# Optimization experiments

Measured on AMD Instinct MI355X. Metric: run time of the kernel, lower is better.

The kernel has to match this reference:

```python
import jax, jax.numpy as jnp
import numpy as np

N = 100000      # num_nodes
R = 8           # num_relations
D = 128         # hidden_dim
E = 600000      # num_edges
P = 100000      # num query pairs
PH = 128        # pair_hidden_dim


def _xavier(key, shape):
    fan_in, fan_out = shape[-2], shape[-1]
    limit = float(np.sqrt(6.0 / (fan_in + fan_out)))
    return jax.random.uniform(key, shape, jnp.float32, -limit, limit)


def setup_inputs() -> dict:
    key = jax.random.key(0)
    ks = jax.random.split(key, 16)
    edge_index = jax.random.randint(ks[0], (2, E), 0, N)
    edge_type = jax.random.randint(ks[1], (E,), 0, R)
    drug_index = jax.random.randint(ks[2], (P,), 0, N)
    disease_index = jax.random.randint(ks[3], (P,), 0, N)
    emb = _xavier(ks[4], (N, D))
    rw1 = _xavier(ks[5], (R, D, D))
    sl1 = _xavier(ks[6], (D, D))
    b1 = jnp.zeros((D,), jnp.float32)
    rw2 = _xavier(ks[7], (R, D, D))
    sl2 = _xavier(ks[8], (D, D))
    b2 = jnp.zeros((D,), jnp.float32)
    pw1 = _xavier(ks[9], (3 * D, PH))
    pb1 = jnp.zeros((PH,), jnp.float32)
    pw2 = _xavier(ks[10], (PH, 1))
    pb2 = jnp.zeros((1,), jnp.float32)
    return {
        "edge_index": edge_index, "edge_type": edge_type,
        "drug_index": drug_index, "disease_index": disease_index,
        "emb": emb, "rw1": rw1, "sl1": sl1, "b1": b1,
        "rw2": rw2, "sl2": sl2, "b2": b2,
        "pw1": pw1, "pb1": pb1, "pw2": pw2, "pb2": pb2,
    }


def _rgcn_layer(x, rel_w, self_w, bias, src, dst, etype):
    # Transform all node features once per relation: [R, N, D]
    xW = jnp.einsum('nd,rde->rne', x, rel_w)
    # Per-relation in-degree of dst (matches torch bincount-per-relation, clamp_min(1))
    seg_key = etype * N + dst                                  # [E]
    deg = jax.ops.segment_sum(jnp.ones((src.shape[0],), x.dtype), seg_key,
                              num_segments=R * N)
    deg = jnp.maximum(deg, 1.0)
    msg = xW[etype, src] / deg[seg_key][:, None]               # [E, D]
    agg = jax.ops.segment_sum(msg, dst, num_segments=N)        # [N, D]
    return x @ self_w + agg + bias


def reference(edge_index, edge_type, drug_index, disease_index,
              emb, rw1, sl1, b1, rw2, sl2, b2, pw1, pb1, pw2, pb2):
    src, dst = edge_index[0], edge_index[1]
    # encode (eval mode: dropout is identity)
    x = _rgcn_layer(emb, rw1, sl1, b1, src, dst, edge_type)
    x = jax.nn.relu(x)
    x = _rgcn_layer(x, rw2, sl2, b2, src, dst, edge_type)
    # score_pairs
    dh = x[drug_index]
    sh = x[disease_index]
    feat = jnp.concatenate((dh, sh, dh * sh), axis=-1)         # [P, 3D]
    h = jax.nn.relu(feat @ pw1 + pb1)
    logits = (h @ pw2 + pb2)[:, 0]                             # [P]
    return logits
```

## Files before the change

### kernel.cpp

```cpp
#include <hip/hip_runtime.h>

#define D 128
#define RMAX 16

typedef short s16x8 __attribute__((ext_vector_type(8)));
typedef float f32x4 __attribute__((ext_vector_type(4)));

__device__ inline unsigned short f2b(float f) {
    unsigned u = __builtin_bit_cast(unsigned, f);
    unsigned r = (u + 0x7FFFu + ((u >> 16) & 1u)) >> 16;
    return (unsigned short)r;
}
__device__ inline float b2f(unsigned short h) {
    unsigned u = ((unsigned)h) << 16;
    return __builtin_bit_cast(float, u);
}


__global__ void k_count2(const int* __restrict__ etype, const int* __restrict__ srcA,
                         const int* __restrict__ dstA, int E, int N, int R,
                         int* __restrict__ deg, int* __restrict__ srcCnt,
                         int* __restrict__ counts) {
    __shared__ int lh[RMAX];
    if (threadIdx.x < RMAX) lh[threadIdx.x] = 0;
    __syncthreads();
    int e = blockIdx.x * blockDim.x + threadIdx.x;
    if (e < E) {
        int r = etype[e];
        atomicAdd(&deg[r * N + dstA[e]], 1);
        atomicAdd(&srcCnt[r * N + srcA[e]], 1);
        atomicAdd(&lh[r], 1);
    }
    __syncthreads();
    if (threadIdx.x < R && lh[threadIdx.x])
        atomicAdd(&counts[threadIdx.x], lh[threadIdx.x]);
}

__global__ void k_offsets(const int* __restrict__ counts, int* __restrict__ po,
                          int R, int N) {
    if (threadIdx.x == 0 && blockIdx.x == 0) {
        int acc = 0;
        for (int r = 0; r < R; ++r) {
            po[r] = acc;
            acc += ((counts[r] + 127) / 128) * 128;
        }
        po[R] = acc;
        acc += ((N + 127) / 128) * 128;
        po[R + 1] = acc;
    }
}


template<int VPT>
__global__ void k_scan_blk(const int* __restrict__ in, int* __restrict__ tmp,
                           int* __restrict__ bsum, int n) {
    __shared__ int sd[256];
    int t = threadIdx.x;
    long base = (long)blockIdx.x * (256 * VPT) + (long)t * VPT;
    int s[VPT];
    int tsum = 0;
    #pragma unroll
    for (int k = 0; k < VPT; ++k) { s[k] = (base + k < n) ? in[base + k] : 0; tsum += s[k]; }
    sd[t] = tsum;
    __syncthreads();
    for (int off = 1; off < 256; off <<= 1) {
        int v = (t >= off) ? sd[t - off] : 0;
        __syncthreads();
        sd[t] += v;
        __syncthreads();
    }
    int run = sd[t] - tsum;
    #pragma unroll
    for (int k = 0; k < VPT; ++k) { if (base + k < n) tmp[base + k] = run; run += s[k]; }
    if (t == 255) bsum[blockIdx.x] = sd[255];
}

__global__ void k_scanD1(const int* __restrict__ deg, int* __restrict__ tmp,
                         int* __restrict__ bsum, int N, int R) {
    __shared__ int sd[256];
    int t = threadIdx.x;
    long base = (long)blockIdx.x * 1024 + (long)t * 4;
    int s[4];
    int tsum = 0;
    #pragma unroll
    for (int k = 0; k < 4; ++k) {
        int v = 0;
        long d = base + k;
        if (d < N) {
            v = 1;
            for (int r = 0; r < R; ++r) v += deg[(size_t)r * N + d];
        }
        s[k] = v; tsum += v;
    }
    sd[t] = tsum;
    __syncthreads();
    for (int off = 1; off < 256; off <<= 1) {
        int v = (t >= off) ? sd[t - off] : 0;
        __syncthreads();
        sd[t] += v;
        __syncthreads();
    }
    int run = sd[t] - tsum;
    #pragma unroll
    for (int k = 0; k < 4; ++k) { if (base + k < N) tmp[base + k] = run; run += s[k]; }
    if (t == 255) bsum[blockIdx.x] = sd[255];
}

__global__ void k_scan2(const int* __restrict__ bsum, int* __restrict__ boff, int nb,
                        int* __restrict__ tail, int tailval) {
    __shared__ int sd[256];
    int t = threadIdx.x;
    int v = (t < nb) ? bsum[t] : 0;
    sd[t] = v;
    __syncthreads();
    for (int off = 1; off < 256; off <<= 1) {
        int w = (t >= off) ? sd[t - off] : 0;
        __syncthreads();
        sd[t] += w;
        __syncthreads();
    }
    if (t < nb) boff[t] = sd[t] - v;
    if (t == 0 && tail) *tail = tailval;
}

__global__ void k_scan3(const int* __restrict__ tmp, const int* __restrict__ boff,
                        int* __restrict__ out, int n, int shift) {
    int i = blockIdx.x * 256 + threadIdx.x;
    if (i < n) out[i] = tmp[i] + boff[i >> shift];
}


__global__ void k_scatter3(const int* __restrict__ etype, const int* __restrict__ srcA,
                           const int* __restrict__ dstA, int E, int N, int R,
                           const int* __restrict__ srcOff, const int* __restrict__ po,
                           const int* __restrict__ rowstart, const int* __restrict__ deg,
                           int* __restrict__ srcCur, int* __restrict__ cur2,
                           int* __restrict__ slotSrc, float* __restrict__ slotScale,
                           int* __restrict__ red_idx) {
    int t = blockIdx.x * 256 + threadIdx.x;
    if (t < E) {
        int r = etype[t];
        int s = srcA[t], d = dstA[t];
        int bin = r * N + s;
        int rank = atomicAdd(&srcCur[bin], 1);
        int pos = po[r] + (srcOff[bin] - srcOff[r * N]) + rank;
        int rank2 = atomicAdd(&cur2[d], 1);
        slotSrc[pos] = s;
        slotScale[pos] = 1.0f / (float)deg[r * N + d];
        red_idx[rowstart[d] + 1 + rank2] = pos;
    } else if (t < E + N) {
        int n = t - E;
        int pos = po[R] + n;
        slotSrc[pos] = n;
        slotScale[pos] = 1.0f;
        red_idx[rowstart[n]] = pos;
    }
}


__global__ void k_prep(const float* __restrict__ emb,
                       const float* __restrict__ rw1, const float* __restrict__ sl1,
                       const float* __restrict__ rw2, const float* __restrict__ sl2,
                       const float* __restrict__ pw1,
                       unsigned short* __restrict__ embb,
                       unsigned short* __restrict__ wAll1,
                       unsigned short* __restrict__ wAll2,
                       unsigned short* __restrict__ pw1T,
                       int N, int R)
{
    long t = (long)blockIdx.x * 256 + threadIdx.x;
    long u0 = (long)N * D / 4;
    if (t < u0) {
        long i = t * 4;
        f32x4 v = *(const f32x4*)(emb + i);
        unsigned a0 = (unsigned)f2b(v[0]) | ((unsigned)f2b(v[1]) << 16);
        unsigned a1 = (unsigned)f2b(v[2]) | ((unsigned)f2b(v[3]) << 16);
        uint2 o; o.x = a0; o.y = a1;
        *(uint2*)(embb + i) = o;
        return;
    }
    t -= u0;
    long uW = (long)(R + 1) * D * D;
    if (t < 2 * uW) {
        const float* rw = (t < uW) ? rw1 : rw2;
        const float* sl = (t < uW) ? sl1 : sl2;
        unsigned short* o = (t < uW) ? wAll1 : wAll2;
        long u = (t < uW) ? t : t - uW;
        int r = (int)(u >> 14);
        int nb = (int)(u & 16383);
        int n = nb >> 7, kk = nb & 127;
        int ke = kk ^ ((n & 7) << 3);
        float v = (r < R) ? rw[((size_t)r * D + ke) * D + n] : sl[(size_t)ke * D + n];
        o[u] = f2b(v);
        return;
    }
    t -= 2 * uW;
    if (t < 3 * D * D) {
        int n = (int)(t / 384), ck = (int)(t - n * 384);
        int ch = ck >> 7, kl = (ck & 127) ^ ((n & 7) << 3);
        pw1T[t] = f2b(pw1[(size_t)(ch * 128 + kl) * 128 + n]);
    }
}


__global__ __launch_bounds__(256) void k_gemm_msg(
    const unsigned short* __restrict__ xb,
    const unsigned short* __restrict__ wAll,
    const int* __restrict__ slotSrc, const float* __restrict__ slotScale,
    const int* __restrict__ po, int R,
    unsigned short* __restrict__ y)
{
    __shared__ unsigned char smB[32768];
    __shared__ float sscale[128];
    int tid = threadIdx.x;
    int row0 = blockIdx.x * 128;
    if (row0 >= po[R + 1]) return;
    int r = 0;
    while (row0 >= po[r + 1]) ++r;

    int lane = tid & 63, wid = tid >> 6;
    int lo = lane & 15, hi = lane >> 4;

    int r0g = wid * 32 + lo, r1g = r0g + 16;
    int sv0 = slotSrc[row0 + r0g];
    int sv1 = slotSrc[row0 + r1g];
    const unsigned short* xrow0 = xb + (size_t)sv0 * D;
    const unsigned short* xrow1 = xb + (size_t)sv1 * D;
    s16x8 a0[4], a1[4];
    #pragma unroll
    for (int ks = 0; ks < 4; ++ks) {
        a0[ks] = *(const s16x8*)(xrow0 + ks * 32 + hi * 8);
        a1[ks] = *(const s16x8*)(xrow1 + ks * 32 + hi * 8);
    }

    if (tid < 128) sscale[tid] = slotScale[row0 + tid];

    {
        const int4* src = (const int4*)(wAll + (size_t)r * D * D);
        int4* dstl = (int4*)smB;
        #pragma unroll
        for (int i = 0; i < 8; ++i) dstl[tid + i * 256] = src[tid + i * 256];
    }
    __syncthreads();

    f32x4 acc[2][8];
    #pragma unroll
    for (int a = 0; a < 2; ++a)
        #pragma unroll
        for (int b = 0; b < 8; ++b) acc[a][b] = (f32x4){0, 0, 0, 0};

    #pragma unroll
    for (int ks = 0; ks < 4; ++ks) {
        int kb = ks * 64 + hi * 16;
        #pragma unroll
        for (int n = 0; n < 8; ++n) {
            int cr = n * 16 + lo;
            s16x8 bf = *(const s16x8*)(smB + cr * 256 + (kb ^ ((cr & 7) << 4)));
            acc[0][n] = __builtin_amdgcn_mfma_f32_16x16x32_bf16(a0[ks], bf, acc[0][n], 0, 0, 0);
            acc[1][n] = __builtin_amdgcn_mfma_f32_16x16x32_bf16(a1[ks], bf, acc[1][n], 0, 0, 0);
        }
    }

    __syncthreads();
    #pragma unroll
    for (int m2 = 0; m2 < 2; ++m2) {
        int rbase = wid * 32 + m2 * 16 + hi * 4;
        #pragma unroll
        for (int reg = 0; reg < 4; ++reg) {
            int rl = rbase + reg;
            float s = sscale[rl];
            #pragma unroll
            for (int n = 0; n < 8; ++n) {
                int byteoff = rl * 256 + (((n * 32 + (lo >> 3) * 16) ^ ((rl & 7) << 4)) + (lo & 7) * 2);
                *(unsigned short*)(smB + byteoff) = f2b(acc[m2][n][reg] * s);
            }
        }
    }
    __syncthreads();
    {
        int m = tid >> 1, half = tid & 1;
        unsigned short* dst = y + (size_t)(row0 + m) * D;
        #pragma unroll
        for (int i = 0; i < 8; ++i) {
            int c = half * 8 + i;
            int4 v = *(const int4*)(smB + m * 256 + ((c * 16) ^ ((m & 7) << 4)));
            *(int4*)(dst + c * 8) = v;
        }
    }
}


template<bool RELU>
__global__ void k_reduce(const unsigned short* __restrict__ y,
                         const int* __restrict__ red_idx,
                         const int* __restrict__ rowstart,
                         const float* __restrict__ bias,
                         unsigned short* __restrict__ out, int N)
{
    int tid = threadIdx.x;
    int dl = tid >> 4, cj = tid & 15;
    float b[8];
    *(f32x4*)(b)     = *(const f32x4*)(bias + cj * 8);
    *(f32x4*)(b + 4) = *(const f32x4*)(bias + cj * 8 + 4);
    int dbase = blockIdx.x * 64 + dl * 4;
    for (int i = 0; i < 4; ++i) {
        int d = dbase + i;
        if (d >= N) return;
        int s = rowstart[d], e = rowstart[d + 1];
        float a[8];
        #pragma unroll
        for (int j = 0; j < 8; ++j) a[j] = b[j];
        for (int q = s; q < e; ++q) {
            int pos = red_idx[q];
            int4 v = *(const int4*)(y + (size_t)pos * D + cj * 8);
            const unsigned short* hp = (const unsigned short*)&v;
            #pragma unroll
            for (int j = 0; j < 8; ++j) a[j] += b2f(hp[j]);
        }
        unsigned short o[8];
        #pragma unroll
        for (int j = 0; j < 8; ++j) {
            float v = RELU ? fmaxf(a[j], 0.0f) : a[j];
            o[j] = f2b(v);
        }
        *(int4*)(out + (size_t)d * D + cj * 8) = *(const int4*)o;
    }
}


__global__ __launch_bounds__(256) void k_score(
    const unsigned short* __restrict__ x2b,
    const int* __restrict__ drug, const int* __restrict__ dis,
    const unsigned short* __restrict__ pw1T,
    const float* __restrict__ pb1, const float* __restrict__ pw2,
    const float* __restrict__ pb2, float* __restrict__ outp, int P)
{
    __shared__ unsigned char smA[32768];
    __shared__ unsigned char smB[32768];
    __shared__ float pb1s[128];
    __shared__ float pw2s[128];
    int tid = threadIdx.x;
    long p0 = (long)blockIdx.x * 128;
    if (tid < 128) { pb1s[tid] = pb1[tid]; pw2s[tid] = pw2[tid]; }
    float pb2v = pb2[0];

    int lane = tid & 63, wid = tid >> 6;
    int lo = lane & 15, hi = lane >> 4;
    f32x4 acc[2][8];
    #pragma unroll
    for (int a = 0; a < 2; ++a)
        #pragma unroll
        for (int b = 0; b < 8; ++b) acc[a][b] = (f32x4){0, 0, 0, 0};

    for (int ch = 0; ch < 3; ++ch) {
        {
            const int4* src = (const int4*)pw1T;
            int4* dstl = (int4*)smB;
            #pragma unroll
            for (int i = 0; i < 8; ++i) {
                int q = tid + i * 256;
                int n = q >> 4, c = q & 15;
                dstl[q] = src[n * 48 + ch * 16 + c];
            }
        }
        {
            int m = tid >> 1, half = tid & 1;
            long p = p0 + m;
            int4 z = {0, 0, 0, 0};
            if (p < P) {
                const int4* da = (const int4*)(x2b + (size_t)drug[p] * D);
                const int4* db = (const int4*)(x2b + (size_t)dis[p] * D);
                for (int c = half * 8; c < half * 8 + 8; ++c) {
                    int4 v;
                    if (ch == 0) v = da[c];
                    else if (ch == 1) v = db[c];
                    else {
                        int4 va = da[c], vb = db[c];
                        const unsigned short* ap = (const unsigned short*)&va;
                        const unsigned short* bp = (const unsigned short*)&vb;
                        unsigned short o[8];
                        #pragma unroll
                        for (int j = 0; j < 8; ++j) o[j] = f2b(b2f(ap[j]) * b2f(bp[j]));
                        v = *(const int4*)o;
                    }
                    *(int4*)(smA + m * 256 + ((c * 16) ^ ((m & 7) << 4))) = v;
                }
            } else {
                for (int c = half * 8; c < half * 8 + 8; ++c)
                    *(int4*)(smA + m * 256 + ((c * 16) ^ ((m & 7) << 4))) = z;
            }
        }
        __syncthreads();

        #pragma unroll
        for (int ks = 0; ks < 4; ++ks) {
            int kb = ks * 64 + hi * 16;
            int r0 = wid * 32 + lo, r1 = r0 + 16;
            s16x8 a0 = *(const s16x8*)(smA + r0 * 256 + (kb ^ ((r0 & 7) << 4)));
            s16x8 a1 = *(const s16x8*)(smA + r1 * 256 + (kb ^ ((r1 & 7) << 4)));
            #pragma unroll
            for (int n = 0; n < 8; ++n) {
                int cr = n * 16 + lo;
                s16x8 bf = *(const s16x8*)(smB + cr * 256 + (kb ^ ((cr & 7) << 4)));
                acc[0][n] = __builtin_amdgcn_mfma_f32_16x16x32_bf16(a0, bf, acc[0][n], 0, 0, 0);
                acc[1][n] = __builtin_amdgcn_mfma_f32_16x16x32_bf16(a1, bf, acc[1][n], 0, 0, 0);
            }
        }
        __syncthreads();
    }

    #pragma unroll
    for (int m2 = 0; m2 < 2; ++m2)
        #pragma unroll
        for (int reg = 0; reg < 4; ++reg) {
            float s = 0.0f;
            #pragma unroll
            for (int n = 0; n < 8; ++n) {
                int col = n * 16 + lo;
                float v = acc[m2][n][reg] + pb1s[col];
                v = fmaxf(v, 0.0f);
                s = fmaf(v, pw2s[col], s);
            }
            s += __shfl_xor(s, 1, 64);
            s += __shfl_xor(s, 2, 64);
            s += __shfl_xor(s, 4, 64);
            s += __shfl_xor(s, 8, 64);
            long p = p0 + wid * 32 + m2 * 16 + hi * 4 + reg;
            if (lo == 0 && p < P) outp[p] = s + pb2v;
        }
}


extern "C" void kernel_launch(void* const* d_in, const int* in_sizes, int n_in,
                              void* d_out, int out_size, void* d_ws, size_t ws_size,
                              hipStream_t stream) {
    const int*   edge_index = (const int*)d_in[0];
    const int*   edge_type  = (const int*)d_in[1];
    const int*   drug       = (const int*)d_in[2];
    const int*   dis        = (const int*)d_in[3];
    const float* emb        = (const float*)d_in[4];
    const float* rw1        = (const float*)d_in[5];
    const float* sl1        = (const float*)d_in[6];
    const float* b1         = (const float*)d_in[7];
    const float* rw2        = (const float*)d_in[8];
    const float* sl2        = (const float*)d_in[9];
    const float* b2         = (const float*)d_in[10];
    const float* pw1        = (const float*)d_in[11];
    const float* pb1        = (const float*)d_in[12];
    const float* pw2        = (const float*)d_in[13];
    const float* pb2        = (const float*)d_in[14];

    const int E = in_sizes[1];
    const int P = in_sizes[2];
    const int N = in_sizes[4] / D;
    const int R = in_sizes[5] / (D * D);

    const int* srcA = edge_index;
    const int* dstA = edge_index + E;

    const int slotN = E + N + 128 * (R + 1);

    char* ws = (char*)d_ws;
    unsigned short* embb = (unsigned short*)ws; ws += (size_t)N * D * 2;
    unsigned short* x1b  = (unsigned short*)ws; ws += (size_t)N * D * 2;
    unsigned short* y    = (unsigned short*)ws; ws += (size_t)slotN * D * 2;
    unsigned short* wAll1 = (unsigned short*)ws; ws += (size_t)(R + 1) * D * D * 2;
    unsigned short* wAll2 = (unsigned short*)ws; ws += (size_t)(R + 1) * D * D * 2;
    unsigned short* pw1T  = (unsigned short*)ws; ws += (size_t)3 * D * D * 2;
    int*   deg     = (int*)ws;   ws += (size_t)R * N * 4;
    int*   srcCnt  = (int*)ws;   ws += (size_t)R * N * 4;
    int*   srcCur  = (int*)ws;   ws += (size_t)R * N * 4;
    int*   cur2    = (int*)ws;   ws += (size_t)N * 4;
    int*   counts  = (int*)ws;   ws += 256;
    int*   slotSrc = (int*)ws;   ws += (size_t)slotN * 4;
    float* slotScale = (float*)ws; ws += (size_t)slotN * 4;
    size_t zbytes = (size_t)(3 * R * N + N + 64 + 2 * slotN) * 4;
    int*   red_idx = (int*)ws;   ws += (size_t)(E + N) * 4;
    int* srcOff  = (int*)ws; ws += (size_t)R * N * 4;
    int* dtmp    = (int*)ws; ws += (size_t)N * 4;
    int* rowstart = (int*)ws; ws += (size_t)(N + 1) * 4;
    int* bsumS   = (int*)ws; ws += 256 * 4;
    int* boffS   = (int*)ws; ws += 256 * 4;
    int* bsumD   = (int*)ws; ws += 256 * 4;
    int* boffD   = (int*)ws; ws += 256 * 4;
    int* po      = (int*)ws; ws += 256;
    unsigned short* x2b = embb;

    hipMemsetAsync(deg, 0, zbytes, stream);

    long u0 = (long)N * D / 4;
    long uW = (long)(R + 1) * D * D;
    long utot = u0 + 2 * uW + 3 * D * D;
    k_prep<<<(int)((utot + 255) / 256), 256, 0, stream>>>(emb, rw1, sl1, rw2, sl2, pw1,
                                                          embb, wAll1, wAll2, pw1T, N, R);

    k_count2<<<(E + 255) / 256, 256, 0, stream>>>(edge_type, srcA, dstA, E, N, R,
                                                  deg, srcCnt, counts);
    k_offsets<<<1, 1, 0, stream>>>(counts, po, R, N);

    int nbS = (R * N + 4095) / 4096;
    k_scan_blk<16><<<nbS, 256, 0, stream>>>(srcCnt, srcOff, bsumS, R * N);
    k_scan2<<<1, 256, 0, stream>>>(bsumS, boffS, nbS, nullptr, 0);
    k_scan3<<<(R * N + 255) / 256, 256, 0, stream>>>(srcOff, boffS, srcOff, R * N, 12);

    int nbD = (N + 1023) / 1024;
    k_scanD1<<<nbD, 256, 0, stream>>>(deg, dtmp, bsumD, N, R);
    k_scan2<<<1, 256, 0, stream>>>(bsumD, boffD, nbD, rowstart + N, E + N);
    k_scan3<<<(N + 255) / 256, 256, 0, stream>>>(dtmp, boffD, rowstart, N, 10);

    k_scatter3<<<(E + N + 255) / 256, 256, 0, stream>>>(edge_type, srcA, dstA, E, N, R,
                                                        srcOff, po, rowstart, deg,
                                                        srcCur, cur2,
                                                        slotSrc, slotScale, red_idx);

    int gridM = (E + 127) / 128 + (N + 127) / 128 + R + 2;
    int gridR = (N + 63) / 64;

    k_gemm_msg<<<gridM, 256, 0, stream>>>(embb, wAll1, slotSrc, slotScale, po, R, y);
    k_reduce<true><<<gridR, 256, 0, stream>>>(y, red_idx, rowstart, b1, x1b, N);
    k_gemm_msg<<<gridM, 256, 0, stream>>>(x1b, wAll2, slotSrc, slotScale, po, R, y);
    k_reduce<false><<<gridR, 256, 0, stream>>>(y, red_idx, rowstart, b2, x2b, N);
    k_score<<<(P + 127) / 128, 256, 0, stream>>>(x2b, drug, dis, pw1T, pb1, pw2, pb2,
                                                 (float*)d_out, P);
}
```

Baseline: 538.5 us.

## Sort message slots by (relation, dst) and apply degree normalization in reduce

Message slots are now ordered by relation and destination instead of relation and source, so each destination's messages sit contiguously and the reduce kernel walks them using deg/degOff directly. This removes the separate source-count pass, the second scan, the red_idx indirection and the slotScale array, and moves the 1/deg scaling out of the GEMM epilogue into the reduce. In exchange, the GEMM's gathered source rows become random rather than grouped by source, and the reduce loops over all R relations per node with extra degree loads.

```diff
diff --git a/kernel.cpp b/kernel.cpp
--- a/kernel.cpp
+++ b/kernel.cpp
@@ -17,10 +17,9 @@
 }
 
 
-__global__ void k_count2(const int* __restrict__ etype, const int* __restrict__ srcA,
-                         const int* __restrict__ dstA, int E, int N, int R,
-                         int* __restrict__ deg, int* __restrict__ srcCnt,
-                         int* __restrict__ counts) {
+__global__ void k_count2(const int* __restrict__ etype, const int* __restrict__ dstA,
+                         int E, int N, int R,
+                         int* __restrict__ deg, int* __restrict__ counts) {
     __shared__ int lh[RMAX];
     if (threadIdx.x < RMAX) lh[threadIdx.x] = 0;
     __syncthreads();
@@ -28,7 +27,6 @@
     if (e < E) {
         int r = etype[e];
         atomicAdd(&deg[r * N + dstA[e]], 1);
-        atomicAdd(&srcCnt[r * N + srcA[e]], 1);
         atomicAdd(&lh[r], 1);
     }
     __syncthreads();
@@ -75,39 +73,7 @@
     if (t == 255) bsum[blockIdx.x] = sd[255];
 }
 
-__global__ void k_scanD1(const int* __restrict__ deg, int* __restrict__ tmp,
-                         int* __restrict__ bsum, int N, int R) {
-    __shared__ int sd[256];
-    int t = threadIdx.x;
-    long base = (long)blockIdx.x * 1024 + (long)t * 4;
-    int s[4];
-    int tsum = 0;
-    #pragma unroll
-    for (int k = 0; k < 4; ++k) {
-        int v = 0;
-        long d = base + k;
-        if (d < N) {
-            v = 1;
-            for (int r = 0; r < R; ++r) v += deg[(size_t)r * N + d];
-        }
-        s[k] = v; tsum += v;
-    }
-    sd[t] = tsum;
-    __syncthreads();
-    for (int off = 1; off < 256; off <<= 1) {
-        int v = (t >= off) ? sd[t - off] : 0;
-        __syncthreads();
-        sd[t] += v;
-        __syncthreads();
-    }
-    int run = sd[t] - tsum;
-    #pragma unroll
-    for (int k = 0; k < 4; ++k) { if (base + k < N) tmp[base + k] = run; run += s[k]; }
-    if (t == 255) bsum[blockIdx.x] = sd[255];
-}
-
-__global__ void k_scan2(const int* __restrict__ bsum, int* __restrict__ boff, int nb,
-                        int* __restrict__ tail, int tailval) {
+__global__ void k_scan2(const int* __restrict__ bsum, int* __restrict__ boff, int nb) {
     __shared__ int sd[256];
     int t = threadIdx.x;
     int v = (t < nb) ? bsum[t] : 0;
@@ -120,7 +86,6 @@
         __syncthreads();
     }
     if (t < nb) boff[t] = sd[t] - v;
-    if (t == 0 && tail) *tail = tailval;
 }
 
 __global__ void k_scan3(const int* __restrict__ tmp, const int* __restrict__ boff,
@@ -132,28 +97,18 @@
 
 __global__ void k_scatter3(const int* __restrict__ etype, const int* __restrict__ srcA,
                            const int* __restrict__ dstA, int E, int N, int R,
-                           const int* __restrict__ srcOff, const int* __restrict__ po,
-                           const int* __restrict__ rowstart, const int* __restrict__ deg,
-                           int* __restrict__ srcCur, int* __restrict__ cur2,
-                           int* __restrict__ slotSrc, float* __restrict__ slotScale,
-                           int* __restrict__ red_idx) {
+                           const int* __restrict__ degOff, const int* __restrict__ po,
+                           int* __restrict__ binCur, int* __restrict__ slotSrc) {
     int t = blockIdx.x * 256 + threadIdx.x;
     if (t < E) {
         int r = etype[t];
-        int s = srcA[t], d = dstA[t];
-        int bin = r * N + s;
-        int rank = atomicAdd(&srcCur[bin], 1);
-        int pos = po[r] + (srcOff[bin] - srcOff[r * N]) + rank;
-        int rank2 = atomicAdd(&cur2[d], 1);
-        slotSrc[pos] = s;
-        slotScale[pos] = 1.0f / (float)deg[r * N + d];
-        red_idx[rowstart[d] + 1 + rank2] = pos;
+        int bin = r * N + dstA[t];
+        int rank = atomicAdd(&binCur[bin], 1);
+        int pos = po[r] + (degOff[bin] - degOff[r * N]) + rank;
+        slotSrc[pos] = srcA[t];
     } else if (t < E + N) {
         int n = t - E;
-        int pos = po[R] + n;
-        slotSrc[pos] = n;
-        slotScale[pos] = 1.0f;
-        red_idx[rowstart[n]] = pos;
+        slotSrc[po[R] + n] = n;
     }
 }
 
@@ -206,12 +161,11 @@
 __global__ __launch_bounds__(256) void k_gemm_msg(
     const unsigned short* __restrict__ xb,
     const unsigned short* __restrict__ wAll,
-    const int* __restrict__ slotSrc, const float* __restrict__ slotScale,
+    const int* __restrict__ slotSrc,
     const int* __restrict__ po, int R,
     unsigned short* __restrict__ y)
 {
     __shared__ unsigned char smB[32768];
-    __shared__ float sscale[128];
     int tid = threadIdx.x;
     int row0 = blockIdx.x * 128;
     if (row0 >= po[R + 1]) return;
@@ -233,8 +187,6 @@
         a1[ks] = *(const s16x8*)(xrow1 + ks * 32 + hi * 8);
     }
 
-    if (tid < 128) sscale[tid] = slotScale[row0 + tid];
-
     {
         const int4* src = (const int4*)(wAll + (size_t)r * D * D);
         int4* dstl = (int4*)smB;
@@ -268,11 +220,10 @@
         #pragma unroll
         for (int reg = 0; reg < 4; ++reg) {
             int rl = rbase + reg;
-            float s = sscale[rl];
             #pragma unroll
             for (int n = 0; n < 8; ++n) {
                 int byteoff = rl * 256 + (((n * 32 + (lo >> 3) * 16) ^ ((rl & 7) << 4)) + (lo & 7) * 2);
-                *(unsigned short*)(smB + byteoff) = f2b(acc[m2][n][reg] * s);
+                *(unsigned short*)(smB + byteoff) = f2b(acc[m2][n][reg]);
             }
         }
     }
@@ -291,31 +242,49 @@
 
 
 template<bool RELU>
-__global__ void k_reduce(const unsigned short* __restrict__ y,
-                         const int* __restrict__ red_idx,
-                         const int* __restrict__ rowstart,
-                         const float* __restrict__ bias,
-                         unsigned short* __restrict__ out, int N)
+__global__ void k_reduce2(const unsigned short* __restrict__ y,
+                          const int* __restrict__ deg, const int* __restrict__ degOff,
+                          const int* __restrict__ po,
+                          const float* __restrict__ bias,
+                          unsigned short* __restrict__ out, int N, int R)
 {
+    __shared__ int rbase[RMAX + 1];
     int tid = threadIdx.x;
-    int dl = tid >> 4, cj = tid & 15;
+    if (tid <= R) rbase[tid] = (tid < R) ? (po[tid] - degOff[(size_t)tid * N]) : po[R];
+    __syncthreads();
+
+    int team = tid >> 4, cj = tid & 15;
     float b[8];
     *(f32x4*)(b)     = *(const f32x4*)(bias + cj * 8);
     *(f32x4*)(b + 4) = *(const f32x4*)(bias + cj * 8 + 4);
-    int dbase = blockIdx.x * 64 + dl * 4;
+    int dbase = blockIdx.x * 64 + team * 4;
     for (int i = 0; i < 4; ++i) {
         int d = dbase + i;
         if (d >= N) return;
-        int s = rowstart[d], e = rowstart[d + 1];
         float a[8];
-        #pragma unroll
-        for (int j = 0; j < 8; ++j) a[j] = b[j];
-        for (int q = s; q < e; ++q) {
-            int pos = red_idx[q];
-            int4 v = *(const int4*)(y + (size_t)pos * D + cj * 8);
+        {
+            int4 v = *(const int4*)(y + (size_t)(rbase[R] + d) * D + cj * 8);
             const unsigned short* hp = (const unsigned short*)&v;
             #pragma unroll
-            for (int j = 0; j < 8; ++j) a[j] += b2f(hp[j]);
+            for (int j = 0; j < 8; ++j) a[j] = b[j] + b2f(hp[j]);
+        }
+        for (int r = 0; r < R; ++r) {
+            int bin = r * N + d;
+            int len = deg[bin];
+            if (!len) continue;
+            long start = rbase[r] + degOff[bin];
+            float s8[8];
+            #pragma unroll
+            for (int j = 0; j < 8; ++j) s8[j] = 0.0f;
+            for (int q = 0; q < len; ++q) {
+                int4 v = *(const int4*)(y + (size_t)(start + q) * D + cj * 8);
+                const unsigned short* hp = (const unsigned short*)&v;
+                #pragma unroll
+                for (int j = 0; j < 8; ++j) s8[j] += b2f(hp[j]);
+            }
+            float inv = 1.0f / (float)len;
+            #pragma unroll
+            for (int j = 0; j < 8; ++j) a[j] = fmaf(s8[j], inv, a[j]);
         }
         unsigned short o[8];
         #pragma unroll
@@ -468,21 +437,13 @@
     unsigned short* wAll2 = (unsigned short*)ws; ws += (size_t)(R + 1) * D * D * 2;
     unsigned short* pw1T  = (unsigned short*)ws; ws += (size_t)3 * D * D * 2;
     int*   deg     = (int*)ws;   ws += (size_t)R * N * 4;
-    int*   srcCnt  = (int*)ws;   ws += (size_t)R * N * 4;
-    int*   srcCur  = (int*)ws;   ws += (size_t)R * N * 4;
-    int*   cur2    = (int*)ws;   ws += (size_t)N * 4;
+    int*   binCur  = (int*)ws;   ws += (size_t)R * N * 4;
     int*   counts  = (int*)ws;   ws += 256;
     int*   slotSrc = (int*)ws;   ws += (size_t)slotN * 4;
-    float* slotScale = (float*)ws; ws += (size_t)slotN * 4;
-    size_t zbytes = (size_t)(3 * R * N + N + 64 + 2 * slotN) * 4;
-    int*   red_idx = (int*)ws;   ws += (size_t)(E + N) * 4;
-    int* srcOff  = (int*)ws; ws += (size_t)R * N * 4;
-    int* dtmp    = (int*)ws; ws += (size_t)N * 4;
-    int* rowstart = (int*)ws; ws += (size_t)(N + 1) * 4;
-    int* bsumS   = (int*)ws; ws += 256 * 4;
-    int* boffS   = (int*)ws; ws += 256 * 4;
-    int* bsumD   = (int*)ws; ws += 256 * 4;
-    int* boffD   = (int*)ws; ws += 256 * 4;
+    size_t zbytes = (size_t)(2 * R * N + 64 + slotN) * 4;
+    int* degOff  = (int*)ws; ws += (size_t)R * N * 4;
+    int* bsum    = (int*)ws; ws += 256 * 4;
+    int* boff    = (int*)ws; ws += 256 * 4;
     int* po      = (int*)ws; ws += 256;
     unsigned short* x2b = embb;
 
@@ -494,32 +455,24 @@
     k_prep<<<(int)((utot + 255) / 256), 256, 0, stream>>>(emb, rw1, sl1, rw2, sl2, pw1,
                                                           embb, wAll1, wAll2, pw1T, N, R);
 
-    k_count2<<<(E + 255) / 256, 256, 0, stream>>>(edge_type, srcA, dstA, E, N, R,
-                                                  deg, srcCnt, counts);
+    k_count2<<<(E + 255) / 256, 256, 0, stream>>>(edge_type, dstA, E, N, R, deg, counts);
     k_offsets<<<1, 1, 0, stream>>>(counts, po, R, N);
 
     int nbS = (R * N + 4095) / 4096;
-    k_scan_blk<16><<<nbS, 256, 0, stream>>>(srcCnt, srcOff, bsumS, R * N);
-    k_scan2<<<1, 256, 0, stream>>>(bsumS, boffS, nbS, nullptr, 0);
-    k_scan3<<<(R * N + 255) / 256, 256, 0, stream>>>(srcOff, boffS, srcOff, R * N, 12);
-
-    int nbD = (N + 1023) / 1024;
-    k_scanD1<<<nbD, 256, 0, stream>>>(deg, dtmp, bsumD, N, R);
-    k_scan2<<<1, 256, 0, stream>>>(bsumD, boffD, nbD, rowstart + N, E + N);
-    k_scan3<<<(N + 255) / 256, 256, 0, stream>>>(dtmp, boffD, rowstart, N, 10);
+    k_scan_blk<16><<<nbS, 256, 0, stream>>>(deg, degOff, bsum, R * N);
+    k_scan2<<<1, 256, 0, stream>>>(bsum, boff, nbS);
+    k_scan3<<<(R * N + 255) / 256, 256, 0, stream>>>(degOff, boff, degOff, R * N, 12);
 
     k_scatter3<<<(E + N + 255) / 256, 256, 0, stream>>>(edge_type, srcA, dstA, E, N, R,
-                                                        srcOff, po, rowstart, deg,
-                                                        srcCur, cur2,
-                                                        slotSrc, slotScale, red_idx);
+                                                        degOff, po, binCur, slotSrc);
 
     int gridM = (E + 127) / 128 + (N + 127) / 128 + R + 2;
     int gridR = (N + 63) / 64;
 
-    k_gemm_msg<<<gridM, 256, 0, stream>>>(embb, wAll1, slotSrc, slotScale, po, R, y);
-    k_reduce<true><<<gridR, 256, 0, stream>>>(y, red_idx, rowstart, b1, x1b, N);
-    k_gemm_msg<<<gridM, 256, 0, stream>>>(x1b, wAll2, slotSrc, slotScale, po, R, y);
-    k_reduce<false><<<gridR, 256, 0, stream>>>(y, red_idx, rowstart, b2, x2b, N);
+    k_gemm_msg<<<gridM, 256, 0, stream>>>(embb, wAll1, slotSrc, po, R, y);
+    k_reduce2<true><<<gridR, 256, 0, stream>>>(y, deg, degOff, po, b1, x1b, N, R);
+    k_gemm_msg<<<gridM, 256, 0, stream>>>(x1b, wAll2, slotSrc, po, R, y);
+    k_reduce2<false><<<gridR, 256, 0, stream>>>(y, deg, degOff, po, b2, x2b, N, R);
     k_score<<<(P + 127) / 128, 256, 0, stream>>>(x2b, drug, dis, pw1T, pb1, pw2, pb2,
                                                  (float*)d_out, P);
 }
```

Result: faster. 508.3 us (-5.6%).
